# Performance work log

Hardware: AMD Instinct MI355X
Metric: run time of the kernel (lower is better)

## Reference

```python
import jax, jax.numpy as jnp
import numpy as np

B, S, D, H = 2, 4096, 512, 8
HD = D // H  # head_dim = 64


def setup_inputs() -> dict:
    key = jax.random.key(0)
    ks = jax.random.split(key, 12)
    scale = 0.02
    inp = {
        "q": jax.random.normal(ks[0], (B, S, D), dtype=jnp.float32),
        "k": jax.random.normal(ks[1], (B, S, D), dtype=jnp.float32),
        "v": jax.random.normal(ks[2], (B, S, D), dtype=jnp.float32),
        "mask": jax.random.randint(ks[3], (B, S, S), 0, 2, dtype=jnp.int32),
        "wq_kernel": jax.random.normal(ks[4], (D, D), dtype=jnp.float32) * scale,
        "wq_bias": jnp.zeros((D,), dtype=jnp.float32),
        "wk_kernel": jax.random.normal(ks[5], (D, D), dtype=jnp.float32) * scale,
        "wk_bias": jnp.zeros((D,), dtype=jnp.float32),
        "wv_kernel": jax.random.normal(ks[6], (D, D), dtype=jnp.float32) * scale,
        "wv_bias": jnp.zeros((D,), dtype=jnp.float32),
        "wo_kernel": jax.random.normal(ks[7], (D, D), dtype=jnp.float32) * scale,
        "wo_bias": jnp.zeros((D,), dtype=jnp.float32),
    }
    return inp


def reference(q, k, v, mask, wq_kernel, wq_bias, wk_kernel, wk_bias,
              wv_kernel, wv_bias, wo_kernel, wo_bias):
    # Dense projections
    qp = q @ wq_kernel + wq_bias            # [B,S,D]
    kp = k @ wk_kernel + wk_bias
    vp = v @ wv_kernel + wv_bias

    def split_heads(x):
        # [B,S,D] -> [B,H,S,HD]
        return x.reshape(B, S, H, HD).transpose(0, 2, 1, 3)

    qh, kh, vh = split_heads(qp), split_heads(kp), split_heads(vp)

    # Scaled dot-product attention (materializes full [B,H,S,S] scores,
    # faithful to the original unfused implementation's math)
    scores = jnp.einsum('bhqd,bhkd->bhqk', qh, kh) / jnp.sqrt(
        jnp.asarray(HD, dtype=jnp.float32))
    scores = scores + mask.astype(jnp.float32)[:, None, :, :] * (-1e9)
    attn = jax.nn.softmax(scores, axis=-1)
    out = jnp.einsum('bhqk,bhkd->bhqd', attn, vh)   # [B,H,S,HD]

    # merge heads: [B,H,S,HD] -> [B,S,D]
    out = out.transpose(0, 2, 1, 3).reshape(B, S, D)
    return out @ wo_kernel + wo_bias
```

## Files before the change

### kernel.cpp

```cpp
#include <hip/hip_runtime.h>
#include <stdint.h>

#define B_ 2
#define S_ 4096
#define D_ 512
#define H_ 8
#define HD_ 64
#define M_ (B_*S_)

typedef __attribute__((ext_vector_type(8))) short bf16x8;
typedef __attribute__((ext_vector_type(4))) float f32x4;

#define QSCALE (0.125f * 1.44269504088896341f)
#define MFMA16(A,B,C) __builtin_amdgcn_mfma_f32_16x16x32_bf16((A),(B),(C),0,0,0)

__device__ __forceinline__ unsigned short f2bf(float f) {
  union { float f; unsigned u; } un; un.f = f;
  unsigned u = un.u;
  return (unsigned short)((u + 0x7fffu + ((u >> 16) & 1u)) >> 16);
}

__device__ __forceinline__ unsigned cvtpk(float lo, float hi) {
  unsigned r;
  asm("v_cvt_pk_bf16_f32 %0, %1, %2" : "=v"(r) : "v"(lo), "v"(hi));
  return r;
}

__device__ __forceinline__ void gl16(const void* g, void* l) {
  __builtin_amdgcn_global_load_lds(
      (const __attribute__((address_space(1))) void*)g,
      (__attribute__((address_space(3))) void*)l, 16, 0, 0);
}

__device__ __forceinline__ int kperm_inv(int p) {
  return ((p & 0x1C) << 1) | ((p & 0x20) >> 3) | (p & 3);
}

__global__ __launch_bounds__(256) void mpack(const int* __restrict__ mask,
                                             unsigned long long* __restrict__ bits) {
  const int nw = (gridDim.x * 256) >> 6;
  int w = (blockIdx.x * 256 + threadIdx.x) >> 6;
  int lane = threadIdx.x & 63;
  const int NWORD = (int)((size_t)B_ * S_ * S_ / 64);
  for (int word = w; word < NWORD; word += nw) {
    int m = mask[(size_t)word * 64 + lane];
    unsigned long long bal = __ballot(m != 0);
    if (lane == 0) bits[word] = bal;
  }
}

__global__ __launch_bounds__(256) void wtrans4(const float* __restrict__ w0, const float* __restrict__ w1,
                                               const float* __restrict__ w2, const float* __restrict__ w3,
                                               unsigned short* __restrict__ t0, unsigned short* __restrict__ t1,
                                               unsigned short* __restrict__ t2, unsigned short* __restrict__ t3) {
  const float* W = blockIdx.z==0?w0: blockIdx.z==1?w1: blockIdx.z==2?w2:w3;
  unsigned short* T = blockIdx.z==0?t0: blockIdx.z==1?t1: blockIdx.z==2?t2:t3;
  __shared__ float tile[32][33];
  int n0 = blockIdx.x*32, k0 = blockIdx.y*32;
  int tx = threadIdx.x & 31, ty = threadIdx.x >> 5;
  #pragma unroll
  for (int i=0;i<4;i++)
    tile[ty + i*8][tx] = W[(size_t)(k0 + ty + i*8)*D_ + n0 + tx];
  __syncthreads();
  #pragma unroll
  for (int i=0;i<4;i++)
    T[(size_t)(n0 + ty + i*8)*D_ + k0 + tx] = f2bf(tile[tx][ty + i*8]);
}

template<int OUT_MODE, int CONVA>
__device__ __forceinline__ void gemm_body(const void* __restrict__ Ap,
                                          const unsigned short* __restrict__ Wt,
                                          const float* __restrict__ bias,
                                          void* __restrict__ Out, float oscale) {
  __shared__ __align__(16) unsigned short lAB[2*128*64];
  unsigned short* lA = lAB;
  unsigned short* lB = lAB + 128*64;
  int bm = blockIdx.x, bn = blockIdx.y;
  int tid = threadIdx.x, lane = tid & 63, wid = tid >> 6;
  int g = lane >> 4, cc = lane & 15;
  int wm = wid >> 1, wn = wid & 1;

  f32x4 acc[4][4];
  #pragma unroll
  for (int mi=0;mi<4;mi++)
    #pragma unroll
    for (int ni=0;ni<4;ni++)
      acc[mi][ni] = (f32x4){0.f,0.f,0.f,0.f};

  for (int ks = 0; ks < D_; ks += 64) {
    __syncthreads();
    #pragma unroll
    for (int c4 = 0; c4 < 4; c4++) {
      int idx = wid*256 + c4*64 + lane;
      int row = idx >> 3, ch = idx & 7;
      int sw = ch ^ (row & 7);
      bf16x8 va;
      if (CONVA) {
        const float* a32 = (const float*)Ap + (size_t)(bm*128 + row)*D_ + ks + ch*8;
        float4 f0 = *(const float4*)a32;
        float4 f1 = *(const float4*)(a32 + 4);
        union { unsigned d[4]; bf16x8 v; } u;
        u.d[0] = cvtpk(f0.x, f0.y);
        u.d[1] = cvtpk(f0.z, f0.w);
        u.d[2] = cvtpk(f1.x, f1.y);
        u.d[3] = cvtpk(f1.z, f1.w);
        va = u.v;
      } else {
        va = *(const bf16x8*)((const unsigned short*)Ap + (size_t)(bm*128 + row)*D_ + ks + ch*8);
      }
      bf16x8 vb = *(const bf16x8*)(Wt + (size_t)(bn*128 + row)*D_ + ks + ch*8);
      *(bf16x8*)((char*)lA + row*128 + sw*16) = va;
      *(bf16x8*)((char*)lB + row*128 + sw*16) = vb;
    }
    __syncthreads();
    #pragma unroll
    for (int kk = 0; kk < 2; kk++) {
      bf16x8 af[4], bfv[4];
      #pragma unroll
      for (int mi=0;mi<4;mi++) {
        int row = wm*64 + mi*16 + cc;
        af[mi] = *(const bf16x8*)((const char*)lA + row*128 + (((4*kk+g) ^ (row&7))<<4));
      }
      #pragma unroll
      for (int ni=0;ni<4;ni++) {
        int row = wn*64 + ni*16 + cc;
        bfv[ni] = *(const bf16x8*)((const char*)lB + row*128 + (((4*kk+g) ^ (row&7))<<4));
      }
      #pragma unroll
      for (int mi=0;mi<4;mi++)
        #pragma unroll
        for (int ni=0;ni<4;ni++)
          acc[mi][ni] = MFMA16(af[mi], bfv[ni], acc[mi][ni]);
    }
  }

  if (OUT_MODE == 2) {
    __syncthreads();
    char* ldsT = (char*)lAB + wid*8192;
    #pragma unroll
    for (int ni=0;ni<4;ni++) {
      int n_l = ni*16 + cc;
      float bv = bias[bn*128 + wn*64 + n_l];
      #pragma unroll
      for (int mi=0;mi<4;mi++) {
        ushort4 pk;
        pk.x = f2bf(acc[mi][ni][0] + bv);
        pk.y = f2bf(acc[mi][ni][1] + bv);
        pk.z = f2bf(acc[mi][ni][2] + bv);
        pk.w = f2bf(acc[mi][ni][3] + bv);
        *(ushort4*)(ldsT + n_l*128 + ((32*mi + 8*g) ^ ((n_l&7)<<4))) = pk;
      }
    }
    asm volatile("s_waitcnt lgkmcnt(0)" ::: "memory");
    __builtin_amdgcn_sched_barrier(0);
    #pragma unroll
    for (int it=0; it<8; ++it) {
      int task = it*64 + lane;
      int row = task >> 3, ch = task & 7;
      bf16x8 vv = *(const bf16x8*)(ldsT + row*128 + ((ch ^ (row&7))<<4));
      int n_g = bn*128 + wn*64 + row;
      int m_g = bm*128 + wm*64 + ch*8;
      int bb = m_g >> 12, ss = m_g & (S_-1);
      int hh = n_g >> 6, hd = n_g & 63;
      *(bf16x8*)((unsigned short*)Out + (((size_t)(bb*H_+hh)*HD_ + hd)*S_ + ss)) = vv;
    }
    return;
  }

  #pragma unroll
  for (int ni=0;ni<4;ni++) {
    int n = bn*128 + wn*64 + ni*16 + cc;
    float bv = bias[n];
    #pragma unroll
    for (int mi=0;mi<4;mi++) {
      f32x4 vacc = acc[mi][ni];
      #pragma unroll
      for (int j=0;j<4;j++) {
        int r = bm*128 + wm*64 + mi*16 + 4*g + j;
        float val = (vacc[j] + bv) * oscale;
        if (OUT_MODE == 0) {
          int b = r >> 12, s = r & (S_-1);
          int h = n >> 6, hd = n & 63;
          ((unsigned short*)Out)[(((size_t)(b*H_ + h)*S_ + s) << 6) + hd] = f2bf(val);
        } else {
          ((float*)Out)[(size_t)r*D_ + n] = val;
        }
      }
    }
  }
}

__global__ __launch_bounds__(256,3) void qkv_gemm(
    const float* __restrict__ q32, const float* __restrict__ k32, const float* __restrict__ v32,
    const unsigned short* __restrict__ wqt, const unsigned short* __restrict__ wkt,
    const unsigned short* __restrict__ wvt,
    const float* __restrict__ bq, const float* __restrict__ bk, const float* __restrict__ bv,
    unsigned short* __restrict__ Qp, unsigned short* __restrict__ Kp,
    unsigned short* __restrict__ Vt) {
  if (blockIdx.z == 0)      gemm_body<0,1>(q32, wqt, bq, Qp, QSCALE);
  else if (blockIdx.z == 1) gemm_body<0,1>(k32, wkt, bk, Kp, 1.0f);
  else                      gemm_body<2,1>(v32, wvt, bv, Vt, 1.0f);
}

__global__ __launch_bounds__(256,3) void o_gemm(const unsigned short* __restrict__ att,
                                                const unsigned short* __restrict__ wot,
                                                const float* __restrict__ bo,
                                                float* __restrict__ out) {
  gemm_body<1,0>(att, wot, bo, out, 1.0f);
}


#define WAITBAR { asm volatile("s_waitcnt vmcnt(6)" ::: "memory"); \
                  __builtin_amdgcn_s_barrier(); }

#define ISSUE(SLOT, TIDX) { \
    int tn_ = (TIDX) < NT ? (TIDX) : NT-1; \
    char* kb_ = lds + (SLOT)*8192 + woff; \
    char* vb_ = lds + 32768 + (SLOT)*8192 + woff; \
    gl16(gkA + (size_t)tn_*(64*HD_), kb_); \
    gl16(gkB + (size_t)tn_*(64*HD_), kb_ + 4096); \
    gl16(gvA + tn_*64, vb_); \
    gl16(gvB + tn_*64, vb_ + 4096); \
    msk0[SLOT] = mb0p[tn_]; \
    msk1[SLOT] = mb1p[tn_]; }

#define QK(SLOT, S0, S1) { \
    __builtin_amdgcn_s_setprio(1); \
    _Pragma("unroll") \
    for (int t4=0;t4<4;t4++) { \
      bf16x8 ak0 = *(const bf16x8*)(lds + (SLOT)*8192 + rdO[t4][0]); \
      bf16x8 ak1 = *(const bf16x8*)(lds + (SLOT)*8192 + rdO[t4][1]); \
      f32x4 s0 = (f32x4){0.f,0.f,0.f,0.f}; \
      s0 = MFMA16(ak0, aq00, s0); \
      s0 = MFMA16(ak1, aq01, s0); \
      f32x4 s1 = (f32x4){0.f,0.f,0.f,0.f}; \
      s1 = MFMA16(ak0, aq10, s1); \
      s1 = MFMA16(ak1, aq11, s1); \
      S0[t4] = s0; S1[t4] = s1; \
    } \
    __builtin_amdgcn_s_setprio(0); }

#define SMPV(S0, S1, VSLOT, MSLOT) { \
    unsigned long long sh0 = msk0[MSLOT] >> g8, sh1 = msk1[MSLOT] >> g8; \
    unsigned lo0=(unsigned)sh0, hi0=(unsigned)(sh0>>32); \
    unsigned lo1=(unsigned)sh1, hi1=(unsigned)(sh1>>32); \
    union { unsigned d[2][4]; bf16x8 v[2]; } P0_, P1_; \
    _Pragma("unroll") \
    for (int t4=0;t4<4;t4++) { \
      unsigned bm0=(t4&1)?hi0:lo0, bm1=(t4&1)?hi1:lo1; \
      const int bb=(t4>>1)*4; \
      float a0=__builtin_amdgcn_exp2f(S0[t4][0]-mj); \
      float a1=__builtin_amdgcn_exp2f(S0[t4][1]-mj); \
      float a2=__builtin_amdgcn_exp2f(S0[t4][2]-mj); \
      float a3=__builtin_amdgcn_exp2f(S0[t4][3]-mj); \
      a0=(bm0&(1u<<(bb+0)))?0.f:a0; a1=(bm0&(1u<<(bb+1)))?0.f:a1; \
      a2=(bm0&(1u<<(bb+2)))?0.f:a2; a3=(bm0&(1u<<(bb+3)))?0.f:a3; \
      P0_.d[t4&1][(t4>>1)*2]   = cvtpk(a0,a1); \
      P0_.d[t4&1][(t4>>1)*2+1] = cvtpk(a2,a3); \
      float c0=__builtin_amdgcn_exp2f(S1[t4][0]-mj); \
      float c1=__builtin_amdgcn_exp2f(S1[t4][1]-mj); \
      float c2=__builtin_amdgcn_exp2f(S1[t4][2]-mj); \
      float c3=__builtin_amdgcn_exp2f(S1[t4][3]-mj); \
      c0=(bm1&(1u<<(bb+0)))?0.f:c0; c1=(bm1&(1u<<(bb+1)))?0.f:c1; \
      c2=(bm1&(1u<<(bb+2)))?0.f:c2; c3=(bm1&(1u<<(bb+3)))?0.f:c3; \
      P1_.d[t4&1][(t4>>1)*2]   = cvtpk(c0,c1); \
      P1_.d[t4&1][(t4>>1)*2+1] = cvtpk(c2,c3); \
    } \
    __builtin_amdgcn_s_setprio(1); \
    _Pragma("unroll") \
    for (int kk=0;kk<2;kk++) { \
      lj40 = MFMA16(P0_.v[kk], vones, lj40); \
      lj41 = MFMA16(P1_.v[kk], vones, lj41); \
      _Pragma("unroll") \
      for (int t4=0;t4<4;t4++) { \
        bf16x8 bv8 = *(const bf16x8*)(lds + 32768 + (VSLOT)*8192 + rdO[t4][kk]); \
        o20[t4] = MFMA16(P0_.v[kk], bv8, o20[t4]); \
        o21[t4] = MFMA16(P1_.v[kk], bv8, o21[t4]); \
      } \
    } \
    __builtin_amdgcn_s_setprio(0); \
    float pm0 = fmaxf(fmaxf(fmaxf(S0[0][0],S0[0][1]),fmaxf(S0[0][2],S0[0][3])),  \
                fmaxf(fmaxf(fmaxf(S0[1][0],S0[1][1]),fmaxf(S0[1][2],S0[1][3])),  \
                fmaxf(fmaxf(fmaxf(S0[2][0],S0[2][1]),fmaxf(S0[2][2],S0[2][3])),  \
                      fmaxf(fmaxf(S0[3][0],S0[3][1]),fmaxf(S0[3][2],S0[3][3]))))); \
    float pm1 = fmaxf(fmaxf(fmaxf(S1[0][0],S1[0][1]),fmaxf(S1[0][2],S1[0][3])),  \
                fmaxf(fmaxf(fmaxf(S1[1][0],S1[1][1]),fmaxf(S1[1][2],S1[1][3])),  \
                fmaxf(fmaxf(fmaxf(S1[2][0],S1[2][1]),fmaxf(S1[2][2],S1[2][3])),  \
                      fmaxf(fmaxf(S1[3][0],S1[3][1]),fmaxf(S1[3][2],S1[3][3]))))); \
    float pm = fmaxf(pm0, pm1); \
    if (__any(pm > mj + 7.f)) { \
      pm = fmaxf(pm, __shfl_xor(pm, 16)); \
      pm = fmaxf(pm, __shfl_xor(pm, 32)); \
      float mn = fmaxf(mj, pm); \
      float alpha = __builtin_amdgcn_exp2f(mj - mn); \
      mj = mn; \
      _Pragma("unroll") \
      for (int j=0;j<4;j++) { \
        float aj = __shfl(alpha, 4*g + j); \
        lj40[j] *= aj; lj41[j] *= aj; \
        _Pragma("unroll") \
        for (int t4=0;t4<4;t4++) { o20[t4][j] *= aj; o21[t4][j] *= aj; } \
      } \
    } }

__global__ __launch_bounds__(256,2) void fattn(const unsigned short* __restrict__ Qp,
                                               const unsigned short* __restrict__ Kp,
                                               const unsigned short* __restrict__ Vt,
                                               const unsigned long long* __restrict__ bits,
                                               unsigned short* __restrict__ attO) {
  __shared__ __align__(16) char lds[65536];
  const int tid = threadIdx.x, lane = tid & 63, wid = tid >> 6;
  const int g = lane >> 4, cc = lane & 15;
  const int g8 = g << 3;

  const int n = blockIdx.x;
  const int xcd = n & 7, idx = n >> 3;
  const int bh = xcd*2 + (idx >> 5);
  const int qb = idx & 31;
  const int b = bh >> 3;
  const int q0w = qb*128 + wid*32;

  const unsigned short* Qb = Qp + (size_t)bh*S_*HD_;
  const unsigned short* Kb = Kp + (size_t)bh*S_*HD_;
  const unsigned short* Vb = Vt + (size_t)bh*HD_*S_;

  bf16x8 aq00 = *(const bf16x8*)(Qb + (size_t)(q0w+cc)*HD_ + g8);
  bf16x8 aq01 = *(const bf16x8*)(Qb + (size_t)(q0w+cc)*HD_ + 32 + g8);
  bf16x8 aq10 = *(const bf16x8*)(Qb + (size_t)(q0w+16+cc)*HD_ + g8);
  bf16x8 aq11 = *(const bf16x8*)(Qb + (size_t)(q0w+16+cc)*HD_ + 32 + g8);

  int rdO[4][2];
  #pragma unroll
  for (int t4=0;t4<4;t4++) {
    int row = t4*16 + cc;
    int base = row*128 + ((g ^ (row&7)) << 4);
    rdO[t4][0] = base;
    rdO[t4][1] = base ^ 64;
  }

  const int p0 = wid*8 + (lane >> 3);
  const int sl = lane & 7;
  const int cK = sl ^ (p0 & 7);
  const unsigned short* gkA = Kb + (size_t)kperm_inv(p0)      *HD_ + cK*8;
  const unsigned short* gkB = Kb + (size_t)kperm_inv(p0 + 32) *HD_ + cK*8;
  const unsigned short* gvA = Vb + (size_t)p0*S_ + cK*8;
  const unsigned short* gvB = gvA + (size_t)32*S_;
  const int woff = wid*1024;

  const unsigned long long* mb0p = bits + ((size_t)(b*S_ + q0w +      cc)) * (S_/64);
  const unsigned long long* mb1p = bits + ((size_t)(b*S_ + q0w + 16 + cc)) * (S_/64);

  union { unsigned d[4]; bf16x8 v; } onesu;
  onesu.d[0] = onesu.d[1] = onesu.d[2] = onesu.d[3] = 0x3F803F80u;
  const bf16x8 vones = onesu.v;

  f32x4 o20[4], o21[4];
  #pragma unroll
  for (int t4=0;t4<4;t4++) { o20[t4] = (f32x4){0.f,0.f,0.f,0.f}; o21[t4] = (f32x4){0.f,0.f,0.f,0.f}; }
  f32x4 lj40 = (f32x4){0.f,0.f,0.f,0.f};
  f32x4 lj41 = (f32x4){0.f,0.f,0.f,0.f};
  float mj = 0.f;

  unsigned long long msk0[4], msk1[4];
  f32x4 stA0[4], stA1[4], stB0[4], stB1[4];

  const int NT = S_/64;

  ISSUE(0, 0)
  ISSUE(1, 1)

  WAITBAR ISSUE(2, 2) QK(0, stA0, stA1)
  WAITBAR ISSUE(3, 3) QK(1, stB0, stB1) SMPV(stA0, stA1, 0, 0)
  WAITBAR ISSUE(0, 4) QK(2, stA0, stA1) SMPV(stB0, stB1, 1, 1)
  WAITBAR ISSUE(1, 5) QK(3, stB0, stB1) SMPV(stA0, stA1, 2, 2)

  #pragma unroll 1
  for (int t = 4; t < NT; t += 4) {
    WAITBAR ISSUE(2, t+2) QK(0, stA0, stA1) SMPV(stB0, stB1, 3, 3)
    WAITBAR ISSUE(3, t+3) QK(1, stB0, stB1) SMPV(stA0, stA1, 0, 0)
    WAITBAR ISSUE(0, t+4) QK(2, stA0, stA1) SMPV(stB0, stB1, 1, 1)
    WAITBAR ISSUE(1, t+5) QK(3, stB0, stB1) SMPV(stA0, stA1, 2, 2)
  }

  SMPV(stB0, stB1, 3, 3)

  const int h = bh & (H_-1);
  #pragma unroll
  for (int j=0;j<4;j++) {
    float i0 = __builtin_amdgcn_rcpf(lj40[j]);
    float i1 = __builtin_amdgcn_rcpf(lj41[j]);
    int qr0 = q0w + 4*g + j;
    int qr1 = q0w + 16 + 4*g + j;
    unsigned short* orow0 = attO + ((size_t)b*S_ + qr0)*D_ + h*HD_;
    unsigned short* orow1 = attO + ((size_t)b*S_ + qr1)*D_ + h*HD_;
    #pragma unroll
    for (int t4=0;t4<4;t4++) {
      orow0[t4*16 + cc] = f2bf(o20[t4][j] * i0);
      orow1[t4*16 + cc] = f2bf(o21[t4][j] * i1);
    }
  }
}

extern "C" void kernel_launch(void* const* d_in, const int* in_sizes, int n_in,
                              void* d_out, int out_size, void* d_ws, size_t ws_size,
                              hipStream_t stream) {
  const float* q    = (const float*)d_in[0];
  const float* k    = (const float*)d_in[1];
  const float* v    = (const float*)d_in[2];
  const int*   mask = (const int*)  d_in[3];
  const float* wq   = (const float*)d_in[4];
  const float* bq   = (const float*)d_in[5];
  const float* wk   = (const float*)d_in[6];
  const float* bk   = (const float*)d_in[7];
  const float* wv   = (const float*)d_in[8];
  const float* bv   = (const float*)d_in[9];
  const float* wo   = (const float*)d_in[10];
  const float* bo   = (const float*)d_in[11];

  char* ws = (char*)d_ws;
  const size_t SZ_MAT = (size_t)M_ * D_ * 2;
  const size_t SZ_W   = (size_t)D_ * D_ * 2;
  unsigned short* wqt = (unsigned short*)(ws);
  unsigned short* wkt = (unsigned short*)(ws + SZ_W);
  unsigned short* wvt = (unsigned short*)(ws + 2*SZ_W);
  unsigned short* wot = (unsigned short*)(ws + 3*SZ_W);
  unsigned short* Qp  = (unsigned short*)(ws + 4*SZ_W);
  unsigned short* Kp  = (unsigned short*)(ws + 4*SZ_W + SZ_MAT);
  unsigned short* Vt  = (unsigned short*)(ws + 4*SZ_W + 2*SZ_MAT);
  unsigned short* att = (unsigned short*)(ws + 4*SZ_W + 3*SZ_MAT);
  unsigned long long* bits = (unsigned long long*)(ws + 4*SZ_W + 4*SZ_MAT);

  mpack<<<2048, 256, 0, stream>>>(mask, bits);
  wtrans4<<<dim3(16,16,4), 256, 0, stream>>>(wq, wk, wv, wo, wqt, wkt, wvt, wot);
  qkv_gemm<<<dim3(64,4,3), 256, 0, stream>>>(q, k, v, wqt, wkt, wvt,
                                             bq, bk, bv, Qp, Kp, Vt);
  fattn<<<512, 256, 0, stream>>>(Qp, Kp, Vt, bits, att);
  o_gemm<<<dim3(64,4), 256, 0, stream>>>(att, wot, bo, (float*)d_out);
}
```

Baseline: 189.3 us.

## Fuse mask packing into QKV GEMM and restructure attention into double-buffered epochs

Removes the separate mask-packing kernel and folds its bit-ballot loop into the tail of the QKV projection kernel, saving one launch and letting the mask pass overlap the GEMM grid. The flash-attention main loop changes from a 4-slot, one-tile-ahead rotating pipeline with partial vmcnt waits to a 2-slot double buffer. Each epoch now loads two 64-key tiles and waits with vmcnt(0) before a barrier. This simplifies scheduling but reduces the load-compute overlap depth and may expose memory latency in the attention kernel.

```diff
diff --git a/kernel.cpp b/kernel.cpp
--- a/kernel.cpp
+++ b/kernel.cpp
@@ -34,19 +34,6 @@
 
 __device__ __forceinline__ int kperm_inv(int p) {
   return ((p & 0x1C) << 1) | ((p & 0x20) >> 3) | (p & 3);
-}
-
-__global__ __launch_bounds__(256) void mpack(const int* __restrict__ mask,
-                                             unsigned long long* __restrict__ bits) {
-  const int nw = (gridDim.x * 256) >> 6;
-  int w = (blockIdx.x * 256 + threadIdx.x) >> 6;
-  int lane = threadIdx.x & 63;
-  const int NWORD = (int)((size_t)B_ * S_ * S_ / 64);
-  for (int word = w; word < NWORD; word += nw) {
-    int m = mask[(size_t)word * 64 + lane];
-    unsigned long long bal = __ballot(m != 0);
-    if (lane == 0) bits[word] = bal;
-  }
 }
 
 __global__ __launch_bounds__(256) void wtrans4(const float* __restrict__ w0, const float* __restrict__ w1,
@@ -196,10 +183,21 @@
     const unsigned short* __restrict__ wvt,
     const float* __restrict__ bq, const float* __restrict__ bk, const float* __restrict__ bv,
     unsigned short* __restrict__ Qp, unsigned short* __restrict__ Kp,
-    unsigned short* __restrict__ Vt) {
+    unsigned short* __restrict__ Vt,
+    const int* __restrict__ mask, unsigned long long* __restrict__ bits) {
   if (blockIdx.z == 0)      gemm_body<0,1>(q32, wqt, bq, Qp, QSCALE);
   else if (blockIdx.z == 1) gemm_body<0,1>(k32, wkt, bk, Kp, 1.0f);
   else                      gemm_body<2,1>(v32, wvt, bv, Vt, 1.0f);
+
+  const int lin = blockIdx.x + (blockIdx.y << 6) + (blockIdx.z << 8);
+  const int lane = threadIdx.x & 63;
+  int w = (lin * 256 + threadIdx.x) >> 6;
+  const int NWORD = (int)((size_t)B_ * S_ * S_ / 64);
+  for (int word = w; word < NWORD; word += 3072) {
+    int m = mask[(size_t)word * 64 + lane];
+    unsigned long long bal = __ballot(m != 0);
+    if (lane == 0) bits[word] = bal;
+  }
 }
 
 __global__ __launch_bounds__(256,3) void o_gemm(const unsigned short* __restrict__ att,
@@ -210,26 +208,30 @@
 }
 
 
-#define WAITBAR { asm volatile("s_waitcnt vmcnt(6)" ::: "memory"); \
+#define WAITBAR { asm volatile("s_waitcnt vmcnt(0)" ::: "memory"); \
                   __builtin_amdgcn_s_barrier(); }
 
-#define ISSUE(SLOT, TIDX) { \
-    int tn_ = (TIDX) < NT ? (TIDX) : NT-1; \
-    char* kb_ = lds + (SLOT)*8192 + woff; \
-    char* vb_ = lds + 32768 + (SLOT)*8192 + woff; \
-    gl16(gkA + (size_t)tn_*(64*HD_), kb_); \
-    gl16(gkB + (size_t)tn_*(64*HD_), kb_ + 4096); \
-    gl16(gvA + tn_*64, vb_); \
-    gl16(gvB + tn_*64, vb_ + 4096); \
-    msk0[SLOT] = mb0p[tn_]; \
-    msk1[SLOT] = mb1p[tn_]; }
-
-#define QK(SLOT, S0, S1) { \
+#define ISSUE_E(SLOT, E) { \
+    int tn0_ = 2*(E), tn1_ = tn0_ + 1; \
+    char* kb_ = lds + (SLOT)*16384 + woff; \
+    char* vb_ = lds + 32768 + (SLOT)*16384 + woff; \
+    gl16(gkA + (size_t)tn0_*(64*HD_), kb_); \
+    gl16(gkB + (size_t)tn0_*(64*HD_), kb_ + 4096); \
+    gl16(gkA + (size_t)tn1_*(64*HD_), kb_ + 8192); \
+    gl16(gkB + (size_t)tn1_*(64*HD_), kb_ + 8192 + 4096); \
+    gl16(gvA + tn0_*64, vb_); \
+    gl16(gvB + tn0_*64, vb_ + 4096); \
+    gl16(gvA + tn1_*64, vb_ + 8192); \
+    gl16(gvB + tn1_*64, vb_ + 8192 + 4096); \
+    msk0[SLOT][0] = mb0p[tn0_]; msk1[SLOT][0] = mb1p[tn0_]; \
+    msk0[SLOT][1] = mb0p[tn1_]; msk1[SLOT][1] = mb1p[tn1_]; }
+
+#define QK(KOFF, S0, S1) { \
     __builtin_amdgcn_s_setprio(1); \
     _Pragma("unroll") \
     for (int t4=0;t4<4;t4++) { \
-      bf16x8 ak0 = *(const bf16x8*)(lds + (SLOT)*8192 + rdO[t4][0]); \
-      bf16x8 ak1 = *(const bf16x8*)(lds + (SLOT)*8192 + rdO[t4][1]); \
+      bf16x8 ak0 = *(const bf16x8*)(lds + (KOFF) + rdO[t4][0]); \
+      bf16x8 ak1 = *(const bf16x8*)(lds + (KOFF) + rdO[t4][1]); \
       f32x4 s0 = (f32x4){0.f,0.f,0.f,0.f}; \
       s0 = MFMA16(ak0, aq00, s0); \
       s0 = MFMA16(ak1, aq01, s0); \
@@ -240,8 +242,8 @@
     } \
     __builtin_amdgcn_s_setprio(0); }
 
-#define SMPV(S0, S1, VSLOT, MSLOT) { \
-    unsigned long long sh0 = msk0[MSLOT] >> g8, sh1 = msk1[MSLOT] >> g8; \
+#define SMPV(S0, S1, VOFF, MK0, MK1) { \
+    unsigned long long sh0 = (MK0) >> g8, sh1 = (MK1) >> g8; \
     unsigned lo0=(unsigned)sh0, hi0=(unsigned)(sh0>>32); \
     unsigned lo1=(unsigned)sh1, hi1=(unsigned)(sh1>>32); \
     union { unsigned d[2][4]; bf16x8 v[2]; } P0_, P1_; \
@@ -273,7 +275,7 @@
       lj41 = MFMA16(P1_.v[kk], vones, lj41); \
       _Pragma("unroll") \
       for (int t4=0;t4<4;t4++) { \
-        bf16x8 bv8 = *(const bf16x8*)(lds + 32768 + (VSLOT)*8192 + rdO[t4][kk]); \
+        bf16x8 bv8 = *(const bf16x8*)(lds + (VOFF) + rdO[t4][kk]); \
         o20[t4] = MFMA16(P0_.v[kk], bv8, o20[t4]); \
         o21[t4] = MFMA16(P1_.v[kk], bv8, o21[t4]); \
       } \
@@ -303,6 +305,14 @@
       } \
     } }
 
+#define EPOCH(SLOT, E) { \
+    WAITBAR \
+    if ((E)+1 < NE) ISSUE_E((SLOT)^1, (E)+1) \
+    QK((SLOT)*16384,        stA0, stA1) \
+    QK((SLOT)*16384 + 8192, stB0, stB1) \
+    SMPV(stA0, stA1, 32768 + (SLOT)*16384,        msk0[SLOT][0], msk1[SLOT][0]) \
+    SMPV(stB0, stB1, 32768 + (SLOT)*16384 + 8192, msk0[SLOT][1], msk1[SLOT][1]) }
+
 __global__ __launch_bounds__(256,2) void fattn(const unsigned short* __restrict__ Qp,
                                                const unsigned short* __restrict__ Kp,
                                                const unsigned short* __restrict__ Vt,
@@ -361,28 +371,18 @@
   f32x4 lj41 = (f32x4){0.f,0.f,0.f,0.f};
   float mj = 0.f;
 
-  unsigned long long msk0[4], msk1[4];
+  unsigned long long msk0[2][2], msk1[2][2];
   f32x4 stA0[4], stA1[4], stB0[4], stB1[4];
 
-  const int NT = S_/64;
-
-  ISSUE(0, 0)
-  ISSUE(1, 1)
-
-  WAITBAR ISSUE(2, 2) QK(0, stA0, stA1)
-  WAITBAR ISSUE(3, 3) QK(1, stB0, stB1) SMPV(stA0, stA1, 0, 0)
-  WAITBAR ISSUE(0, 4) QK(2, stA0, stA1) SMPV(stB0, stB1, 1, 1)
-  WAITBAR ISSUE(1, 5) QK(3, stB0, stB1) SMPV(stA0, stA1, 2, 2)
+  const int NE = S_/128;
+
+  ISSUE_E(0, 0)
 
   #pragma unroll 1
-  for (int t = 4; t < NT; t += 4) {
-    WAITBAR ISSUE(2, t+2) QK(0, stA0, stA1) SMPV(stB0, stB1, 3, 3)
-    WAITBAR ISSUE(3, t+3) QK(1, stB0, stB1) SMPV(stA0, stA1, 0, 0)
-    WAITBAR ISSUE(0, t+4) QK(2, stA0, stA1) SMPV(stB0, stB1, 1, 1)
-    WAITBAR ISSUE(1, t+5) QK(3, stB0, stB1) SMPV(stA0, stA1, 2, 2)
-  }
-
-  SMPV(stB0, stB1, 3, 3)
+  for (int e = 0; e < NE; e += 2) {
+    EPOCH(0, e)
+    EPOCH(1, e+1)
+  }
 
   const int h = bh & (H_-1);
   #pragma unroll
@@ -430,10 +430,9 @@
   unsigned short* att = (unsigned short*)(ws + 4*SZ_W + 3*SZ_MAT);
   unsigned long long* bits = (unsigned long long*)(ws + 4*SZ_W + 4*SZ_MAT);
 
-  mpack<<<2048, 256, 0, stream>>>(mask, bits);
   wtrans4<<<dim3(16,16,4), 256, 0, stream>>>(wq, wk, wv, wo, wqt, wkt, wvt, wot);
   qkv_gemm<<<dim3(64,4,3), 256, 0, stream>>>(q, k, v, wqt, wkt, wvt,
-                                             bq, bk, bv, Qp, Kp, Vt);
+                                             bq, bk, bv, Qp, Kp, Vt, mask, bits);
   fattn<<<512, 256, 0, stream>>>(Qp, Kp, Vt, bits, att);
   o_gemm<<<dim3(64,4), 256, 0, stream>>>(att, wot, bo, (float*)d_out);
 }
```

Result: slower. 264.7 us (+39.8%).
